# Performance work log

Measured on AMD Instinct MI355X. Metric: run time of the kernel, lower is better.

## Reference

```python
import jax, jax.numpy as jnp
import numpy as np

NEG_SLOPE = 0.01  # torch nn.LeakyReLU default


def _normalize_adj(A):
    """Faithful port of GraphConvolution.adj_normalize for a non-symmetric A.

    torch builds diag_embed(d_s) and does a batched matmul D @ A; that is
    mathematically a row scaling, expressed here as a broadcast multiply.
    """
    B, N, _ = A.shape
    # rows whose (A + A^T) row-sum is nonzero get a self-loop of 1 on the diagonal
    mask = jnp.sum(A + jnp.swapaxes(A, 1, 2), axis=-1) != 0  # [B, N]
    idx = jnp.arange(N)
    diag = A[:, idx, idx]
    A = A.at[:, idx, idx].set(jnp.where(mask, 1.0, diag))
    d = A.sum(-1)  # [B, N] out-degree
    # asymmetric branch: d_s = d^-1 where d != 0 else 0;  D @ A == d_s[:, :, None] * A
    d_inv = jnp.where(d != 0, 1.0 / d, 0.0)
    return d_inv[..., None] * A


def setup_inputs() -> dict:
    key = jax.random.key(0)
    k1, k2, k3 = jax.random.split(key, 3)
    B, N, D_in, D_out = 8, 2048, 128, 128
    x = jax.random.normal(k1, (B, N, D_in), dtype=jnp.float32)
    A = jax.random.uniform(k2, (B, N, N), dtype=jnp.float32)
    W = jax.random.normal(k3, (D_out, D_in), dtype=jnp.float32) * 0.05
    return {"x": x, "A": A, "W": W}


def reference(x, A, W):
    # adj_normalize(...).detach()
    An = jax.lax.stop_gradient(_normalize_adj(A))  # [B, N, N]
    # fc (no bias) + LeakyReLU
    h = jax.nn.leaky_relu(jnp.einsum('bnd,ed->bne', x, W), negative_slope=NEG_SLOPE)
    # dense aggregation A @ h; dropout(p=0) is identity (eval mode)
    return jnp.einsum('bnm,bme->bne', An, h)
```

## Files before the change

kernel.cpp:

```cpp
#include <hip/hip_runtime.h>
#include <hip/hip_bf16.h>

#define BB 8
#define NN 2048
#define DD 128

typedef float f32x4_t __attribute__((ext_vector_type(4)));
typedef short s16x8_t __attribute__((ext_vector_type(8)));

__device__ __forceinline__ unsigned short f2bf(float f){
  union { float f; unsigned int u; } v; v.f = f;
  unsigned int u = v.u;
  u += 0x7FFFu + ((u >> 16) & 1u);
  return (unsigned short)(u >> 16);
}
__device__ __forceinline__ float bf2f(unsigned short s){
  union { unsigned int u; float f; } v; v.u = ((unsigned int)s) << 16;
  return v.f;
}

__global__ __launch_bounds__(256) void gc_phase1(const float* __restrict__ x,
                                                 const float* __restrict__ W,
                                                 unsigned short* __restrict__ h,
                                                 unsigned short* __restrict__ hT){
  __shared__ float smem[64*132 + 128*128];
  float* xs = smem;
  float* WT = smem + 64*132;

  const int t  = threadIdx.x;
  const int b  = blockIdx.y;
  const int m0 = blockIdx.x * 64;

  {
    const int e = t >> 1, d0 = (t & 1) * 64;
    const float* wr = W + e*DD + d0;
    #pragma unroll
    for (int i = 0; i < 64; i += 4){
      float4 wv = *(const float4*)(wr + i);
      WT[(d0+i+0)*128 + e] = wv.x;
      WT[(d0+i+1)*128 + e] = wv.y;
      WT[(d0+i+2)*128 + e] = wv.z;
      WT[(d0+i+3)*128 + e] = wv.w;
    }
  }
  #pragma unroll
  for (int i = 0; i < 8; i++){
    int s = t + i*256;
    int row = s >> 5, c4 = (s & 31) * 4;
    float4 xv = *(const float4*)(x + ((size_t)(b*NN + m0 + row))*DD + c4);
    *(float4*)(xs + row*132 + c4) = xv;
  }
  __syncthreads();

  const int rg = t >> 4, cg = t & 15;
  const int r0 = rg*4, c0 = cg*8;
  float acc[4][8];
  #pragma unroll
  for (int i=0;i<4;i++)
    #pragma unroll
    for (int j=0;j<8;j++) acc[i][j] = 0.f;

  #pragma unroll 4
  for (int d = 0; d < 128; d++){
    float4 wa = *(const float4*)(WT + d*128 + c0);
    float4 wb = *(const float4*)(WT + d*128 + c0 + 4);
    #pragma unroll
    for (int i=0;i<4;i++){
      float xv = xs[(r0+i)*132 + d];
      acc[i][0] += xv*wa.x; acc[i][1] += xv*wa.y;
      acc[i][2] += xv*wa.z; acc[i][3] += xv*wa.w;
      acc[i][4] += xv*wb.x; acc[i][5] += xv*wb.y;
      acc[i][6] += xv*wb.z; acc[i][7] += xv*wb.w;
    }
  }

  unsigned short hb[4][8];
  #pragma unroll
  for (int i=0;i<4;i++){
    s16x8_t st;
    #pragma unroll
    for (int j=0;j<8;j++){
      float v = acc[i][j];
      v = v > 0.f ? v : 0.01f*v;
      hb[i][j] = f2bf(v);
      st[j] = (short)hb[i][j];
    }
    *(s16x8_t*)(h + ((size_t)(b*NN + m0 + r0 + i))*DD + c0) = st;
  }

  __syncthreads();
  unsigned short* Tb = (unsigned short*)smem;
  #pragma unroll
  for (int i=0;i<4;i++)
    #pragma unroll
    for (int j=0;j<8;j++)
      Tb[(c0+j)*72 + (r0+i)] = hb[i][j];
  __syncthreads();

  {
    const int e = t >> 1, mh = (t & 1) * 32;
    unsigned short* dst = hT + ((size_t)(b*DD + e))*NN + m0 + mh;
    #pragma unroll
    for (int i = 0; i < 32; i += 8)
      *(s16x8_t*)(dst + i) = *(const s16x8_t*)(Tb + e*72 + mh + i);
  }
}

__global__ __launch_bounds__(256) void gc_main(const float* __restrict__ A,
                                               const unsigned short* __restrict__ h,
                                               const unsigned short* __restrict__ hT,
                                               float* __restrict__ out){
  __shared__ unsigned short hbuf[2][128*64];

  const int tid = threadIdx.x;
  const int w = tid >> 6, l = tid & 63;
  const int b = blockIdx.y;
  const int rowbase = blockIdx.x * 64;
  const int wm0 = rowbase + w*16;
  const int rl = l & 15, kc = l >> 4;
  const int myrow = wm0 + rl;

  const float* Arow = A + ((size_t)(b*NN + myrow))*NN;
  const float diagv = Arow[myrow];

  const unsigned short* hTb = hT + (size_t)b * DD * NN;
  const int e_base = w*32 + (l >> 3);
  const int csw = (l & 7) ^ (l >> 3);
  const unsigned short* stage_src0 = hTb + (size_t)e_base * NN + csw*8;

  f32x4_t acc[8];
  #pragma unroll
  for (int n=0;n<8;n++) acc[n] = (f32x4_t){0.f,0.f,0.f,0.f};
  float rsum = 0.f;
  float4 ar[4], arn[4];

  auto stage = [&](int bi, int k0){
    #pragma unroll
    for (int q = 0; q < 4; q++){
      const unsigned short* src = stage_src0 + (size_t)q*8*NN + k0;
      unsigned short* dst = &hbuf[bi][(w*32 + q*8)*64];
      __builtin_amdgcn_global_load_lds((const __attribute__((address_space(1))) void*)src,
                                       (__attribute__((address_space(3))) void*)dst,
                                       16, 0, 0);
    }
  };
  auto loadA = [&](float4* r, int k0){
    const float* ap = Arow + k0 + kc*8;
    r[0] = *(const float4*)(ap);
    r[1] = *(const float4*)(ap + 4);
    r[2] = *(const float4*)(ap + 32);
    r[3] = *(const float4*)(ap + 36);
  };

  stage(0, 0);
  loadA(ar, 0);
  __syncthreads();

  for (int t = 0; t < 32; t++){
    const int cur = t & 1;
    if (t < 31){
      stage(cur ^ 1, (t+1)*64);
      loadA(arn, (t+1)*64);
    }
    #pragma unroll
    for (int kk = 0; kk < 2; kk++){
      float4 lo = ar[kk*2], hi = ar[kk*2+1];
      rsum += lo.x+lo.y+lo.z+lo.w + hi.x+hi.y+hi.z+hi.w;
      s16x8_t af;
      af[0]=(short)f2bf(lo.x); af[1]=(short)f2bf(lo.y);
      af[2]=(short)f2bf(lo.z); af[3]=(short)f2bf(lo.w);
      af[4]=(short)f2bf(hi.x); af[5]=(short)f2bf(hi.y);
      af[6]=(short)f2bf(hi.z); af[7]=(short)f2bf(hi.w);
      const int slot = (kk*4 + kc) ^ (rl & 7);
      #pragma unroll
      for (int n = 0; n < 8; n++){
        const int er = n*16 + rl;
        const s16x8_t bf = *(const s16x8_t*)&hbuf[cur][er*64 + slot*8];
        acc[n] = __builtin_amdgcn_mfma_f32_16x16x32_bf16(af, bf, acc[n], 0, 0, 0);
      }
    }
    __syncthreads();
    ar[0]=arn[0]; ar[1]=arn[1]; ar[2]=arn[2]; ar[3]=arn[3];
  }

  rsum += __shfl_xor(rsum, 16);
  rsum += __shfl_xor(rsum, 32);
  const float dval = rsum - diagv + 1.0f;
  const float dinv = 1.0f / dval;
  const float dfac = 1.0f - bf2f(f2bf(diagv));

  const unsigned short* hb_ = h + (size_t)b * NN * DD;
  float* outb = out + (size_t)b * NN * DD;
  #pragma unroll
  for (int j = 0; j < 4; j++){
    const int row_l = kc*4 + j;
    const int rowg = wm0 + row_l;
    const float dj = __shfl(dinv, row_l);
    const float fj = __shfl(dfac, row_l);
    #pragma unroll
    for (int n = 0; n < 8; n++){
      const int col = n*16 + rl;
      const float hv = bf2f(hb_[(size_t)rowg*DD + col]);
      outb[(size_t)rowg*DD + col] = dj * (acc[n][j] + fj * hv);
    }
  }
}

extern "C" void kernel_launch(void* const* d_in, const int* in_sizes, int n_in,
                              void* d_out, int out_size, void* d_ws, size_t ws_size,
                              hipStream_t stream){
  const float* x = (const float*)d_in[0];
  const float* A = (const float*)d_in[1];
  const float* W = (const float*)d_in[2];
  float* out = (float*)d_out;

  unsigned short* h  = (unsigned short*)d_ws;
  unsigned short* hT = h + (size_t)BB*NN*DD;

  dim3 grid(NN/64, BB);
  gc_phase1<<<grid, dim3(256), 0, stream>>>(x, W, h, hT);
  gc_main  <<<grid, dim3(256), 0, stream>>>(A, h, hT, out);
}
```

Baseline: 230.6 us.

## Split-K main kernel across wave pairs, load B directly from global, remap blocks

The aggregation kernel now uses 32-row tiles with two waves per row group, each covering half of K. Partial results are reduced through shared memory, and the grid grows to 512 blocks for more parallelism across CUs. The LDS double-buffered staging of hT is replaced by direct per-lane global loads into registers, with a software prefetch pipeline for A, and the bf16 packing uses the HIP intrinsic. Phase1 vectorises x reads as float4 and both kernels interleave batches in the block index. The trade-off is that B data is no longer shared through LDS, so global and L2 traffic for hT rises, and register pressure goes up.

```diff
diff --git a/kernel.cpp b/kernel.cpp
--- a/kernel.cpp
+++ b/kernel.cpp
@@ -17,6 +17,14 @@
 __device__ __forceinline__ float bf2f(unsigned short s){
   union { unsigned int u; float f; } v; v.u = ((unsigned int)s) << 16;
   return v.f;
+}
+__device__ __forceinline__ s16x8_t pack_bf16_8(const float4 lo, const float4 hi){
+  union { __hip_bfloat162 p[4]; s16x8_t v; } U;
+  U.p[0] = __float22bfloat162_rn(float2{lo.x, lo.y});
+  U.p[1] = __float22bfloat162_rn(float2{lo.z, lo.w});
+  U.p[2] = __float22bfloat162_rn(float2{hi.x, hi.y});
+  U.p[3] = __float22bfloat162_rn(float2{hi.z, hi.w});
+  return U.v;
 }
 
 __global__ __launch_bounds__(256) void gc_phase1(const float* __restrict__ x,
@@ -27,9 +35,10 @@
   float* xs = smem;
   float* WT = smem + 64*132;
 
-  const int t  = threadIdx.x;
-  const int b  = blockIdx.y;
-  const int m0 = blockIdx.x * 64;
+  const int t   = threadIdx.x;
+  const int bid = blockIdx.x;
+  const int b   = bid & 7;
+  const int m0  = (bid >> 3) * 64;
 
   {
     const int e = t >> 1, d0 = (t & 1) * 64;
@@ -60,17 +69,23 @@
     #pragma unroll
     for (int j=0;j<8;j++) acc[i][j] = 0.f;
 
-  #pragma unroll 4
-  for (int d = 0; d < 128; d++){
-    float4 wa = *(const float4*)(WT + d*128 + c0);
-    float4 wb = *(const float4*)(WT + d*128 + c0 + 4);
-    #pragma unroll
-    for (int i=0;i<4;i++){
-      float xv = xs[(r0+i)*132 + d];
-      acc[i][0] += xv*wa.x; acc[i][1] += xv*wa.y;
-      acc[i][2] += xv*wa.z; acc[i][3] += xv*wa.w;
-      acc[i][4] += xv*wb.x; acc[i][5] += xv*wb.y;
-      acc[i][6] += xv*wb.z; acc[i][7] += xv*wb.w;
+  #pragma unroll 2
+  for (int d = 0; d < 128; d += 4){
+    float4 xv[4];
+    #pragma unroll
+    for (int i=0;i<4;i++) xv[i] = *(const float4*)(xs + (r0+i)*132 + d);
+    #pragma unroll
+    for (int dd=0; dd<4; dd++){
+      float4 wa = *(const float4*)(WT + (d+dd)*128 + c0);
+      float4 wb = *(const float4*)(WT + (d+dd)*128 + c0 + 4);
+      #pragma unroll
+      for (int i=0;i<4;i++){
+        float xq = (dd==0)?xv[i].x:(dd==1)?xv[i].y:(dd==2)?xv[i].z:xv[i].w;
+        acc[i][0] += xq*wa.x; acc[i][1] += xq*wa.y;
+        acc[i][2] += xq*wa.z; acc[i][3] += xq*wa.w;
+        acc[i][4] += xq*wb.x; acc[i][5] += xq*wb.y;
+        acc[i][6] += xq*wb.z; acc[i][7] += xq*wb.w;
+      }
     }
   }
 
@@ -106,102 +121,118 @@
   }
 }
 
-__global__ __launch_bounds__(256) void gc_main(const float* __restrict__ A,
-                                               const unsigned short* __restrict__ h,
-                                               const unsigned short* __restrict__ hT,
-                                               float* __restrict__ out){
-  __shared__ unsigned short hbuf[2][128*64];
+#define LOADA(d0_,d1_,d2_,d3_, tt) do {                 \
+    const float* _ap = Arow + k0 + (tt)*64 + kc*8;      \
+    d0_ = *(const float4*)(_ap);                        \
+    d1_ = *(const float4*)(_ap+4);                      \
+    d2_ = *(const float4*)(_ap+32);                     \
+    d3_ = *(const float4*)(_ap+36);                     \
+  } while(0)
+
+__global__ __launch_bounds__(256, 2) void gc_main(const float* __restrict__ A,
+                                                  const unsigned short* __restrict__ h,
+                                                  const unsigned short* __restrict__ hT,
+                                                  float* __restrict__ out){
+  __shared__ float red[2][16*128];
+  __shared__ float rsred[2][16];
 
   const int tid = threadIdx.x;
   const int w = tid >> 6, l = tid & 63;
-  const int b = blockIdx.y;
-  const int rowbase = blockIdx.x * 64;
-  const int wm0 = rowbase + w*16;
+  const int bid = blockIdx.x;
+  const int b  = bid & 7;
+  const int xt = bid >> 3;
+  const int wpair = w & 1;
+  const int khalf = w >> 1;
+  const int wm0 = xt*32 + wpair*16;
   const int rl = l & 15, kc = l >> 4;
   const int myrow = wm0 + rl;
+  const int k0 = khalf * 1024;
 
   const float* Arow = A + ((size_t)(b*NN + myrow))*NN;
-  const float diagv = Arow[myrow];
-
   const unsigned short* hTb = hT + (size_t)b * DD * NN;
-  const int e_base = w*32 + (l >> 3);
-  const int csw = (l & 7) ^ (l >> 3);
-  const unsigned short* stage_src0 = hTb + (size_t)e_base * NN + csw*8;
+
+  const float diagv = (khalf == 0) ? Arow[myrow] : 0.f;
+
+  const unsigned short* Bp[8];
+  #pragma unroll
+  for (int n=0;n<8;n++) Bp[n] = hTb + (size_t)(n*16 + rl)*NN + k0 + kc*8;
 
   f32x4_t acc[8];
   #pragma unroll
   for (int n=0;n<8;n++) acc[n] = (f32x4_t){0.f,0.f,0.f,0.f};
   float rsum = 0.f;
-  float4 ar[4], arn[4];
-
-  auto stage = [&](int bi, int k0){
-    #pragma unroll
-    for (int q = 0; q < 4; q++){
-      const unsigned short* src = stage_src0 + (size_t)q*8*NN + k0;
-      unsigned short* dst = &hbuf[bi][(w*32 + q*8)*64];
-      __builtin_amdgcn_global_load_lds((const __attribute__((address_space(1))) void*)src,
-                                       (__attribute__((address_space(3))) void*)dst,
-                                       16, 0, 0);
-    }
-  };
-  auto loadA = [&](float4* r, int k0){
-    const float* ap = Arow + k0 + kc*8;
-    r[0] = *(const float4*)(ap);
-    r[1] = *(const float4*)(ap + 4);
-    r[2] = *(const float4*)(ap + 32);
-    r[3] = *(const float4*)(ap + 36);
-  };
-
-  stage(0, 0);
-  loadA(ar, 0);
-  __syncthreads();
-
-  for (int t = 0; t < 32; t++){
-    const int cur = t & 1;
-    if (t < 31){
-      stage(cur ^ 1, (t+1)*64);
-      loadA(arn, (t+1)*64);
-    }
-    #pragma unroll
-    for (int kk = 0; kk < 2; kk++){
-      float4 lo = ar[kk*2], hi = ar[kk*2+1];
-      rsum += lo.x+lo.y+lo.z+lo.w + hi.x+hi.y+hi.z+hi.w;
-      s16x8_t af;
-      af[0]=(short)f2bf(lo.x); af[1]=(short)f2bf(lo.y);
-      af[2]=(short)f2bf(lo.z); af[3]=(short)f2bf(lo.w);
-      af[4]=(short)f2bf(hi.x); af[5]=(short)f2bf(hi.y);
-      af[6]=(short)f2bf(hi.z); af[7]=(short)f2bf(hi.w);
-      const int slot = (kk*4 + kc) ^ (rl & 7);
-      #pragma unroll
-      for (int n = 0; n < 8; n++){
-        const int er = n*16 + rl;
-        const s16x8_t bf = *(const s16x8_t*)&hbuf[cur][er*64 + slot*8];
-        acc[n] = __builtin_amdgcn_mfma_f32_16x16x32_bf16(af, bf, acc[n], 0, 0, 0);
-      }
-    }
-    __syncthreads();
-    ar[0]=arn[0]; ar[1]=arn[1]; ar[2]=arn[2]; ar[3]=arn[3];
+
+  float4 a0,a1,a2,a3, b0,b1,b2,b3, p0,p1,p2,p3;
+  LOADA(a0,a1,a2,a3, 0);
+  LOADA(b0,b1,b2,b3, 1);
+  s16x8_t B0[8];
+  #pragma unroll
+  for (int n=0;n<8;n++) B0[n] = *(const s16x8_t*)(Bp[n]);
+
+  for (int t = 0; t < 16; t++){
+    const int tp = (t+2 < 16) ? t+2 : 15;
+    const int tn = (t+1 < 16) ? t+1 : 15;
+    LOADA(p0,p1,p2,p3, tp);
+    s16x8_t B1[8];
+    #pragma unroll
+    for (int n=0;n<8;n++) B1[n] = *(const s16x8_t*)(Bp[n] + t*64 + 32);
+    {
+      float s0 = (a0.x+a0.y)+(a0.z+a0.w);
+      float s1 = (a1.x+a1.y)+(a1.z+a1.w);
+      rsum += s0+s1;
+      s16x8_t af = pack_bf16_8(a0,a1);
+      #pragma unroll
+      for (int n=0;n<8;n++)
+        acc[n] = __builtin_amdgcn_mfma_f32_16x16x32_bf16(af, B0[n], acc[n], 0,0,0);
+    }
+    #pragma unroll
+    for (int n=0;n<8;n++) B0[n] = *(const s16x8_t*)(Bp[n] + tn*64);
+    {
+      float s0 = (a2.x+a2.y)+(a2.z+a2.w);
+      float s1 = (a3.x+a3.y)+(a3.z+a3.w);
+      rsum += s0+s1;
+      s16x8_t af = pack_bf16_8(a2,a3);
+      #pragma unroll
+      for (int n=0;n<8;n++)
+        acc[n] = __builtin_amdgcn_mfma_f32_16x16x32_bf16(af, B1[n], acc[n], 0,0,0);
+    }
+    a0=b0; a1=b1; a2=b2; a3=b3;
+    b0=p0; b1=p1; b2=p2; b3=p3;
   }
 
   rsum += __shfl_xor(rsum, 16);
   rsum += __shfl_xor(rsum, 32);
-  const float dval = rsum - diagv + 1.0f;
-  const float dinv = 1.0f / dval;
-  const float dfac = 1.0f - bf2f(f2bf(diagv));
-
-  const unsigned short* hb_ = h + (size_t)b * NN * DD;
-  float* outb = out + (size_t)b * NN * DD;
-  #pragma unroll
-  for (int j = 0; j < 4; j++){
-    const int row_l = kc*4 + j;
-    const int rowg = wm0 + row_l;
-    const float dj = __shfl(dinv, row_l);
-    const float fj = __shfl(dfac, row_l);
-    #pragma unroll
-    for (int n = 0; n < 8; n++){
-      const int col = n*16 + rl;
-      const float hv = bf2f(hb_[(size_t)rowg*DD + col]);
-      outb[(size_t)rowg*DD + col] = dj * (acc[n][j] + fj * hv);
+
+  if (khalf == 1){
+    float* rb_ = &red[wpair][0];
+    #pragma unroll
+    for (int n=0;n<8;n++)
+      #pragma unroll
+      for (int j=0;j<4;j++)
+        rb_[(kc*4+j)*128 + n*16 + rl] = acc[n][j];
+    if (l < 16) rsred[wpair][l] = rsum;
+  }
+  __syncthreads();
+  if (khalf == 0){
+    const float rall = rsum + rsred[wpair][rl];
+    const float dinv = 1.0f / (rall - diagv + 1.0f);
+    const float dfac = 1.0f - bf2f(f2bf(diagv));
+    const float* rb_ = &red[wpair][0];
+    const unsigned short* hb_ = h + (size_t)b * NN * DD;
+    float* outb = out + (size_t)b * NN * DD;
+    #pragma unroll
+    for (int j = 0; j < 4; j++){
+      const int row_l = kc*4 + j;
+      const int rowg = wm0 + row_l;
+      const float dj = __shfl(dinv, row_l);
+      const float fj = __shfl(dfac, row_l);
+      #pragma unroll
+      for (int n = 0; n < 8; n++){
+        const int col = n*16 + rl;
+        const float part = acc[n][j] + rb_[row_l*128 + col];
+        const float hv = bf2f(hb_[(size_t)rowg*DD + col]);
+        outb[(size_t)rowg*DD + col] = dj * (part + fj * hv);
+      }
     }
   }
 }
@@ -217,7 +248,6 @@
   unsigned short* h  = (unsigned short*)d_ws;
   unsigned short* hT = h + (size_t)BB*NN*DD;
 
-  dim3 grid(NN/64, BB);
-  gc_phase1<<<grid, dim3(256), 0, stream>>>(x, W, h, hT);
-  gc_main  <<<grid, dim3(256), 0, stream>>>(A, h, hT, out);
-}
+  gc_phase1<<<dim3(256), dim3(256), 0, stream>>>(x, W, h, hT);
+  gc_main  <<<dim3(512), dim3(256), 0, stream>>>(A, h, hT, out);
+}
```

Result: slower. 265.7 us (+15.2%).
